# Kernel optimization log

Measured on AMD Instinct MI355X. Metric: run time of the kernel, lower is better.

The kernel has to match this reference:

```python
import jax, jax.numpy as jnp
import numpy as np

C_S, C_V, C_Z, C_OUT = 32, 8, 128, 128
IN_S, IN_V = 28, 37
N_RBF, N_POS = 64, 64
IN_Z = N_RBF * 25 + N_POS          # 1664 raw pairwise-dist RBF + positional feats
N_LAYERS, K = 4, 30
N_NODES = 1024
N_EDGES = N_NODES * K
WEIGHT_NUMEL = C_S*C_S + C_S*C_V + C_V*C_V + C_V*C_S + C_V*C_V  # 1664
LN_EPS = 1e-5
BN_EPS = 1e-5


def _ln(x, g, b):
    m = x.mean(-1, keepdims=True)
    v = x.var(-1, keepdims=True)
    return (x - m) / jnp.sqrt(v + LN_EPS) * g + b


def _tp(xs, xv, sh_s, sh_v, w):
    """FullyConnectedTensorProduct (32x0e+8x1e) x (0e+1e) -> (32x0e+8x1e), per-edge weights w [E, WEIGHT_NUMEL]."""
    E = w.shape[0]
    o = [0]
    def cut(n1, n2):
        ww = w[:, o[0]:o[0] + n1 * n2].reshape(E, n1, n2)
        o[0] += n1 * n2
        return ww
    w1 = cut(C_S, C_S)  # 0e x 0e -> 0e
    w2 = cut(C_S, C_V)  # 0e x 1e -> 1e
    w3 = cut(C_V, C_V)  # 1e x 0e -> 1e
    w4 = cut(C_V, C_S)  # 1e x 1e -> 0e (dot)
    w5 = cut(C_V, C_V)  # 1e x 1e -> 1e (cross)
    # path normalization: 1/sqrt(in1_mul * n_paths_to_output)
    a1 = 1.0 / np.sqrt(2 * C_S)
    a4 = 1.0 / np.sqrt(2 * C_V)
    a2 = 1.0 / np.sqrt(3 * C_S)
    a3 = 1.0 / np.sqrt(3 * C_V)
    a5 = a3
    out_s = a1 * jnp.einsum('e,ei,eij->ej', sh_s, xs, w1) \
          + (a4 / np.sqrt(3.0)) * jnp.einsum('eix,ex,eij->ej', xv, sh_v, w4)
    cross = jnp.cross(xv, sh_v[:, None, :])  # [E, C_V, 3]
    out_v = a2 * jnp.einsum('ei,eij,ex->ejx', xs, w2, sh_v) \
          + a3 * jnp.einsum('e,eix,eij->ejx', sh_s, xv, w3) \
          + (a5 / np.sqrt(2.0)) * jnp.einsum('eix,eij->ejx', cross, w5)
    return out_s, out_v


def _forward(node_raw, edge_raw, edge_vecs, rot,
             ee_w1, ee_b1, ee_w2, ee_b2, ee_w3, ee_b3, ee_ln_g, ee_ln_b,
             ne_ws, ne_wv,
             fc_w1, fc_b1, fc_w2, fc_b2, bn_g, bn_b, bn_vg,
             eu_lin, eu_w1, eu_b1, eu_w2, eu_b2, eu_w3, eu_b3, eu_ln_g, eu_ln_b,
             mu_w, mu_b, lv_w, lv_b, edge_index):
    N = node_raw.shape[0]
    dst, src = edge_index[0], edge_index[1]
    # spherical harmonics, lmax=1, 'component' normalization: Y0 = 1, Y1 = sqrt(3) * unit
    unit = edge_vecs / (jnp.linalg.norm(edge_vecs, axis=-1, keepdims=True) + 1e-8)
    sh_s = jnp.ones(edge_vecs.shape[0], node_raw.dtype)
    sh_v = np.sqrt(3.0) * unit
    # edge embed MLP + LN
    h = jax.nn.relu(edge_raw @ ee_w1 + ee_b1)
    h = jax.nn.relu(h @ ee_w2 + ee_b2)
    ef = _ln(h @ ee_w3 + ee_b3, ee_ln_g, ee_ln_b)
    # node embed: per-irrep (equivariant) linear 28x0e->32x0e, 37x1e->8x1e
    xs = node_raw[:, :IN_S] @ ne_ws
    xv = jnp.einsum('nix,ij->njx', node_raw[:, IN_S:].reshape(N, IN_V, 3), ne_wv)
    cnt = jnp.maximum(jax.ops.segment_sum(jnp.ones_like(src, node_raw.dtype), src, num_segments=N), 1.0)
    for l in range(N_LAYERS):
        # per-edge TP weights from edge features
        w = jax.nn.relu(ef @ fc_w1[l] + fc_b1[l]) @ fc_w2[l] + fc_b2[l]  # [E, WEIGHT_NUMEL]
        ms, mv = _tp(xs[dst], xv[dst], sh_s, sh_v, w)
        ags = jax.ops.segment_sum(ms, src, num_segments=N) / cnt[:, None]
        agv = jax.ops.segment_sum(mv, src, num_segments=N) / cnt[:, None, None]
        xs = xs + ags  # pad is a no-op: in/out irreps identical
        xv = xv + agv
        # e3nn-style BatchNorm (batch statistics)
        xs = (xs - xs.mean(0)) / jnp.sqrt(xs.var(0) + BN_EPS) * bn_g[l] + bn_b[l]
        fn = jnp.mean(jnp.sum(xv ** 2, -1), 0) / 3.0  # per-channel mean component norm
        xv = xv / jnp.sqrt(fn + BN_EPS)[None, :, None] * bn_vg[l][None, :, None]
        # EdgeUpdate
        a = xs @ eu_lin[l]  # scalar part -> h_edge
        e_in = jnp.concatenate([a[dst], a[src], ef], -1)
        u = jax.nn.relu(e_in @ eu_w1[l] + eu_b1[l])
        u = jax.nn.relu(u @ eu_w2[l] + eu_b2[l])
        u = u @ eu_w3[l] + eu_b3[l]
        ef = _ln(ef + u, eu_ln_g[l], eu_ln_b[l])
    # scalarize vectors w.r.t. per-node frames: R^T v
    xv_loc = jnp.einsum('nxy,ncx->ncy', rot, xv)
    feat = jnp.concatenate([xs, xv_loc.reshape(N, -1)], -1)  # [N, 56]
    mu = feat @ mu_w + mu_b
    lv = feat @ lv_w + lv_b
    return jnp.stack([mu, lv])  # [2, N, C_OUT]


def setup_inputs() -> dict:
    key = jax.random.key(0)
    ks = iter(jax.random.split(key, 80))
    def nrm(shape, fan=None):
        s = 1.0 if fan is None else 1.0 / np.sqrt(fan)
        return jax.random.normal(next(ks), shape, jnp.float32) * s
    inp = {}
    inp['node_raw'] = nrm([N_NODES, IN_S + 3 * IN_V])
    inp['edge_raw'] = nrm([N_EDGES, IN_Z])
    inp['edge_vecs'] = nrm([N_EDGES, 3])
    inp['rot'] = jnp.linalg.qr(nrm([N_NODES, 3, 3]))[0]
    inp['edge_index'] = jax.random.randint(next(ks), (2, N_EDGES), 0, N_NODES, jnp.int32)
    inp['ee_w1'] = nrm([IN_Z, C_Z], IN_Z); inp['ee_b1'] = jnp.zeros([C_Z])
    inp['ee_w2'] = nrm([C_Z, C_Z], C_Z);   inp['ee_b2'] = jnp.zeros([C_Z])
    inp['ee_w3'] = nrm([C_Z, C_Z], C_Z);   inp['ee_b3'] = jnp.zeros([C_Z])
    inp['ee_ln_g'] = jnp.ones([C_Z]); inp['ee_ln_b'] = jnp.zeros([C_Z])
    inp['ne_ws'] = nrm([IN_S, C_S], IN_S)
    inp['ne_wv'] = nrm([IN_V, C_V], IN_V)
    L = N_LAYERS
    inp['fc_w1'] = nrm([L, C_Z, C_Z], C_Z); inp['fc_b1'] = jnp.zeros([L, C_Z])
    inp['fc_w2'] = nrm([L, C_Z, WEIGHT_NUMEL], C_Z); inp['fc_b2'] = jnp.zeros([L, WEIGHT_NUMEL])
    inp['bn_g'] = jnp.ones([L, C_S]); inp['bn_b'] = jnp.zeros([L, C_S]); inp['bn_vg'] = jnp.ones([L, C_V])
    inp['eu_lin'] = nrm([L, C_S, C_Z], C_S)
    inp['eu_w1'] = nrm([L, 3 * C_Z, C_Z], 3 * C_Z); inp['eu_b1'] = jnp.zeros([L, C_Z])
    inp['eu_w2'] = nrm([L, C_Z, C_Z], C_Z); inp['eu_b2'] = jnp.zeros([L, C_Z])
    inp['eu_w3'] = nrm([L, C_Z, C_Z], C_Z); inp['eu_b3'] = jnp.zeros([L, C_Z])
    inp['eu_ln_g'] = jnp.ones([L, C_Z]); inp['eu_ln_b'] = jnp.zeros([L, C_Z])
    D = C_S + 3 * C_V
    inp['mu_w'] = nrm([D, C_OUT], D); inp['mu_b'] = jnp.zeros([C_OUT])
    inp['lv_w'] = nrm([D, C_OUT], D); inp['lv_b'] = jnp.zeros([C_OUT])
    return inp


def reference(node_raw, edge_raw, edge_vecs, rot,
              ee_w1, ee_b1, ee_w2, ee_b2, ee_w3, ee_b3, ee_ln_g, ee_ln_b,
              ne_ws, ne_wv,
              fc_w1, fc_b1, fc_w2, fc_b2, bn_g, bn_b, bn_vg,
              eu_lin, eu_w1, eu_b1, eu_w2, eu_b2, eu_w3, eu_b3, eu_ln_g, eu_ln_b,
              mu_w, mu_b, lv_w, lv_b, edge_index):
    return _forward(node_raw, edge_raw, edge_vecs, rot,
                    ee_w1, ee_b1, ee_w2, ee_b2, ee_w3, ee_b3, ee_ln_g, ee_ln_b,
                    ne_ws, ne_wv,
                    fc_w1, fc_b1, fc_w2, fc_b2, bn_g, bn_b, bn_vg,
                    eu_lin, eu_w1, eu_b1, eu_w2, eu_b2, eu_w3, eu_b3, eu_ln_g, eu_ln_b,
                    mu_w, mu_b, lv_w, lv_b, edge_index)
```

## Files before the change

### kernel.cpp

```cpp
#include <hip/hip_runtime.h>
#include <hip/hip_bf16.h>

typedef __hip_bfloat16 bf16;
typedef __attribute__((ext_vector_type(8))) short s16x8;
typedef __attribute__((ext_vector_type(4))) float f32x4;

#define NN 1024
#define NE 30720
#define CS 32
#define CV 8
#define CZ 128
#define INS 28
#define INV 37
#define NRDIM 139
#define INZ 1664
#define WN 1664
#define NL 4

__device__ __forceinline__ float b2f(bf16 x) { return __bfloat162float(x); }
__device__ __forceinline__ bf16 f2b(float x) { return __float2bfloat16(x); }


template<int RELU, int AF32>
__global__ __launch_bounds__(256)
void gemm64(const void* __restrict__ Ap, const bf16* __restrict__ Bf,
            const float* __restrict__ bias, bf16* __restrict__ Cp,
            int M, int K)
{
    __shared__ __align__(16) bf16 la[64 * 40];
    const int bm = blockIdx.x * 64;
    const int tid = threadIdx.x;
    const int lane = tid & 63;
    const int wv = tid >> 6;
    const int lr = tid >> 1;
    const int lc = (tid & 1) * 16;
    const int l15 = lane & 15;
    const int quad = lane >> 4;
    const int K32 = K >> 5;
    f32x4 acc[4][2] = {};
    const bf16*  ga16 = (const bf16*) Ap + (size_t)(bm + lr) * K + lc;
    const float* ga32 = (const float*)Ap + (size_t)(bm + lr) * K + lc;
    for (int k0 = 0; k0 < K; k0 += 32) {
        union { bf16 h[16]; float4 q[2]; } pa;
        if (tid < 128) {
            if (AF32) {
                float4 f0 = *(const float4*)(ga32 + k0);
                float4 f1 = *(const float4*)(ga32 + k0 + 4);
                float4 f2 = *(const float4*)(ga32 + k0 + 8);
                float4 f3 = *(const float4*)(ga32 + k0 + 12);
                pa.h[0]=f2b(f0.x); pa.h[1]=f2b(f0.y); pa.h[2]=f2b(f0.z); pa.h[3]=f2b(f0.w);
                pa.h[4]=f2b(f1.x); pa.h[5]=f2b(f1.y); pa.h[6]=f2b(f1.z); pa.h[7]=f2b(f1.w);
                pa.h[8]=f2b(f2.x); pa.h[9]=f2b(f2.y); pa.h[10]=f2b(f2.z); pa.h[11]=f2b(f2.w);
                pa.h[12]=f2b(f3.x); pa.h[13]=f2b(f3.y); pa.h[14]=f2b(f3.z); pa.h[15]=f2b(f3.w);
            } else {
                pa.q[0] = *(const float4*)(ga16 + k0);
                pa.q[1] = *(const float4*)(ga16 + k0 + 8);
            }
        }
        s16x8 bfr[2];
#pragma unroll
        for (int ni = 0; ni < 2; ni++)
            bfr[ni] = *(const s16x8*)(Bf + (size_t)(((wv * 2 + ni) * K32 + (k0 >> 5)) * 512) + lane * 8);
        __syncthreads();
        if (tid < 128) {
            *(float4*)&la[lr * 40 + lc]     = pa.q[0];
            *(float4*)&la[lr * 40 + lc + 8] = pa.q[1];
        }
        __syncthreads();
        s16x8 af[4];
#pragma unroll
        for (int mi = 0; mi < 4; mi++)
            af[mi] = *(const s16x8*)&la[(mi * 16 + l15) * 40 + quad * 8];
#pragma unroll
        for (int mi = 0; mi < 4; mi++)
#pragma unroll
            for (int ni = 0; ni < 2; ni++)
                acc[mi][ni] = __builtin_amdgcn_mfma_f32_16x16x32_bf16(af[mi], bfr[ni], acc[mi][ni], 0, 0, 0);
    }
#pragma unroll
    for (int ni = 0; ni < 2; ni++) {
        const int col = wv * 32 + ni * 16 + l15;
        const float bv = bias[col];
#pragma unroll
        for (int mi = 0; mi < 4; mi++) {
            const int row0 = bm + mi * 16 + quad * 4;
#pragma unroll
            for (int r = 0; r < 4; r++) {
                float v = acc[mi][ni][r] + bv;
                if (RELU) v = fmaxf(v, 0.f);
                Cp[(size_t)(row0 + r) * CZ + col] = f2b(v);
            }
        }
    }
}

__global__ __launch_bounds__(256)
void mlp2(const bf16* __restrict__ A,
          const bf16* __restrict__ w2f, const float* __restrict__ b2,
          const bf16* __restrict__ w3f, const float* __restrict__ b3,
          const float* __restrict__ g, const float* __restrict__ bb,
          bf16* efb)
{
    __shared__ __align__(16) bf16 s_a[64 * 136];
    __shared__ __align__(16) bf16 s_u[64 * 136];
    __shared__ float s_o[64 * 132];
    const int bm = blockIdx.x * 64;
    const int t = threadIdx.x;
    const int lane = t & 63;
    const int wv = t >> 6;
    const int l15 = lane & 15;
    const int quad = lane >> 4;
    {
        int r = t >> 2, c0 = (t & 3) * 32;
        const float4* s4 = (const float4*)(A + (size_t)(bm + r) * CZ + c0);
        float4* d4 = (float4*)&s_a[r * 136 + c0];
        d4[0] = s4[0]; d4[1] = s4[1]; d4[2] = s4[2]; d4[3] = s4[3];
    }
    __syncthreads();
    s16x8 af[4][4];
#pragma unroll
    for (int mi = 0; mi < 4; mi++)
#pragma unroll
        for (int kk = 0; kk < 4; kk++)
            af[mi][kk] = *(const s16x8*)&s_a[(mi * 16 + l15) * 136 + kk * 32 + quad * 8];
#pragma unroll
    for (int s = 0; s < 2; s++) {
        int n = wv * 32 + s * 16 + l15;
        f32x4 acc[4] = {};
#pragma unroll
        for (int kk = 0; kk < 4; kk++) {
            s16x8 bfr = *(const s16x8*)(w2f + (size_t)(((wv * 2 + s) * 4 + kk) * 512) + lane * 8);
#pragma unroll
            for (int mi = 0; mi < 4; mi++)
                acc[mi] = __builtin_amdgcn_mfma_f32_16x16x32_bf16(af[mi][kk], bfr, acc[mi], 0, 0, 0);
        }
        float bv = b2[n];
#pragma unroll
        for (int mi = 0; mi < 4; mi++)
#pragma unroll
            for (int r = 0; r < 4; r++)
                s_u[(mi * 16 + quad * 4 + r) * 136 + n] = f2b(fmaxf(acc[mi][r] + bv, 0.f));
    }
    __syncthreads();
#pragma unroll
    for (int mi = 0; mi < 4; mi++)
#pragma unroll
        for (int kk = 0; kk < 4; kk++)
            af[mi][kk] = *(const s16x8*)&s_u[(mi * 16 + l15) * 136 + kk * 32 + quad * 8];
#pragma unroll
    for (int s = 0; s < 2; s++) {
        int n = wv * 32 + s * 16 + l15;
        f32x4 acc[4] = {};
#pragma unroll
        for (int kk = 0; kk < 4; kk++) {
            s16x8 bfr = *(const s16x8*)(w3f + (size_t)(((wv * 2 + s) * 4 + kk) * 512) + lane * 8);
#pragma unroll
            for (int mi = 0; mi < 4; mi++)
                acc[mi] = __builtin_amdgcn_mfma_f32_16x16x32_bf16(af[mi][kk], bfr, acc[mi], 0, 0, 0);
        }
        float bv = b3[n];
#pragma unroll
        for (int mi = 0; mi < 4; mi++)
#pragma unroll
            for (int r = 0; r < 4; r++)
                s_o[(mi * 16 + quad * 4 + r) * 132 + n] = acc[mi][r] + bv;
    }
    __syncthreads();
    {
        int row = wv * 16 + (lane >> 2);
        int q = lane & 3;
        int col0 = q * 32;
        size_t gbase = (size_t)(bm + row) * CZ;
        float s = 0.f, s2 = 0.f;
        for (int i = 0; i < 32; i++) {
            float x = s_o[row * 132 + col0 + i];
            s += x; s2 += x * x;
        }
        s  += __shfl_xor(s, 1);  s2 += __shfl_xor(s2, 1);
        s  += __shfl_xor(s, 2);  s2 += __shfl_xor(s2, 2);
        float mean = s * (1.f / 128.f);
        float var  = s2 * (1.f / 128.f) - mean * mean;
        float rstd = rsqrtf(var + 1e-5f);
        for (int i = 0; i < 32; i++) {
            int col = col0 + i;
            float x = s_o[row * 132 + col];
            efb[gbase + col] = f2b((x - mean) * rstd * g[col] + bb[col]);
        }
    }
}

__global__ __launch_bounds__(256)
void eu_fused(bf16* __restrict__ efb,
              const float* __restrict__ adg, const float* __restrict__ asg,
              const int* __restrict__ ei,
              const bf16* __restrict__ w1cf, const float* __restrict__ b1,
              const bf16* __restrict__ w2f, const float* __restrict__ b2,
              const bf16* __restrict__ w3f, const float* __restrict__ b3,
              const float* __restrict__ g, const float* __restrict__ bb)
{
    __shared__ __align__(16) bf16 s_a[64 * 136];
    __shared__ __align__(16) bf16 s_u1[64 * 136];
    __shared__ __align__(16) float s_go[64 * 132];
    bf16* const s_u2 = (bf16*)s_go;
    const int bm = blockIdx.x * 64;
    const int t = threadIdx.x;
    const int lane = t & 63;
    const int wv = t >> 6;
    const int l15 = lane & 15;
    const int quad = lane >> 4;
    {
        int r = t >> 2, c0 = (t & 3) * 32;
        const float4* s4 = (const float4*)(efb + (size_t)(bm + r) * CZ + c0);
        float4* d4 = (float4*)&s_a[r * 136 + c0];
        d4[0] = s4[0]; d4[1] = s4[1]; d4[2] = s4[2]; d4[3] = s4[3];
        int dst = ei[bm + r], src = ei[NE + bm + r];
        const float4* pd = (const float4*)(adg + (size_t)dst * CZ + c0);
        const float4* ps = (const float4*)(asg + (size_t)src * CZ + c0);
        float4* dg = (float4*)&s_go[r * 132 + c0];
#pragma unroll
        for (int k = 0; k < 8; k++) {
            float4 va = pd[k], vb = ps[k];
            dg[k] = make_float4(va.x + vb.x, va.y + vb.y, va.z + vb.z, va.w + vb.w);
        }
    }
    __syncthreads();
    {
        s16x8 af[4][4];
#pragma unroll
        for (int mi = 0; mi < 4; mi++)
#pragma unroll
            for (int kk = 0; kk < 4; kk++)
                af[mi][kk] = *(const s16x8*)&s_a[(mi * 16 + l15) * 136 + kk * 32 + quad * 8];
#pragma unroll
        for (int s = 0; s < 2; s++) {
            int n = wv * 32 + s * 16 + l15;
            f32x4 acc[4] = {};
#pragma unroll
            for (int kk = 0; kk < 4; kk++) {
                s16x8 bfr = *(const s16x8*)(w1cf + (size_t)(((wv * 2 + s) * 4 + kk) * 512) + lane * 8);
#pragma unroll
                for (int mi = 0; mi < 4; mi++)
                    acc[mi] = __builtin_amdgcn_mfma_f32_16x16x32_bf16(af[mi][kk], bfr, acc[mi], 0, 0, 0);
            }
            float bv = b1[n];
#pragma unroll
            for (int mi = 0; mi < 4; mi++)
#pragma unroll
                for (int r = 0; r < 4; r++) {
                    int e = mi * 16 + quad * 4 + r;
                    s_u1[e * 136 + n] = f2b(fmaxf(acc[mi][r] + bv + s_go[e * 132 + n], 0.f));
                }
        }
    }
    __syncthreads();
    {
        s16x8 af[4][4];
#pragma unroll
        for (int mi = 0; mi < 4; mi++)
#pragma unroll
            for (int kk = 0; kk < 4; kk++)
                af[mi][kk] = *(const s16x8*)&s_u1[(mi * 16 + l15) * 136 + kk * 32 + quad * 8];
#pragma unroll
        for (int s = 0; s < 2; s++) {
            int n = wv * 32 + s * 16 + l15;
            f32x4 acc[4] = {};
#pragma unroll
            for (int kk = 0; kk < 4; kk++) {
                s16x8 bfr = *(const s16x8*)(w2f + (size_t)(((wv * 2 + s) * 4 + kk) * 512) + lane * 8);
#pragma unroll
                for (int mi = 0; mi < 4; mi++)
                    acc[mi] = __builtin_amdgcn_mfma_f32_16x16x32_bf16(af[mi][kk], bfr, acc[mi], 0, 0, 0);
            }
            float bv = b2[n];
#pragma unroll
            for (int mi = 0; mi < 4; mi++)
#pragma unroll
                for (int r = 0; r < 4; r++)
                    s_u2[(mi * 16 + quad * 4 + r) * 136 + n] = f2b(fmaxf(acc[mi][r] + bv, 0.f));
        }
    }
    __syncthreads();
    {
        s16x8 af[4][4];
#pragma unroll
        for (int mi = 0; mi < 4; mi++)
#pragma unroll
            for (int kk = 0; kk < 4; kk++)
                af[mi][kk] = *(const s16x8*)&s_u2[(mi * 16 + l15) * 136 + kk * 32 + quad * 8];
        __syncthreads();
#pragma unroll
        for (int s = 0; s < 2; s++) {
            int n = wv * 32 + s * 16 + l15;
            f32x4 acc[4] = {};
#pragma unroll
            for (int kk = 0; kk < 4; kk++) {
                s16x8 bfr = *(const s16x8*)(w3f + (size_t)(((wv * 2 + s) * 4 + kk) * 512) + lane * 8);
#pragma unroll
                for (int mi = 0; mi < 4; mi++)
                    acc[mi] = __builtin_amdgcn_mfma_f32_16x16x32_bf16(af[mi][kk], bfr, acc[mi], 0, 0, 0);
            }
            float bv = b3[n];
#pragma unroll
            for (int mi = 0; mi < 4; mi++)
#pragma unroll
                for (int r = 0; r < 4; r++) {
                    int e = mi * 16 + quad * 4 + r;
                    s_go[e * 132 + n] = acc[mi][r] + bv + b2f(s_a[e * 136 + n]);
                }
        }
    }
    __syncthreads();
    {
        int row = wv * 16 + (lane >> 2);
        int q = lane & 3;
        int col0 = q * 32;
        size_t gbase = (size_t)(bm + row) * CZ;
        float s = 0.f, s2 = 0.f;
        for (int i = 0; i < 32; i++) {
            float x = s_go[row * 132 + col0 + i];
            s += x; s2 += x * x;
        }
        s  += __shfl_xor(s, 1);  s2 += __shfl_xor(s2, 1);
        s  += __shfl_xor(s, 2);  s2 += __shfl_xor(s2, 2);
        float mean = s * (1.f / 128.f);
        float var  = s2 * (1.f / 128.f) - mean * mean;
        float rstd = rsqrtf(var + 1e-5f);
        for (int i = 0; i < 32; i++) {
            int col = col0 + i;
            float x = s_go[row * 132 + col];
            efb[gbase + col] = f2b((x - mean) * rstd * g[col] + bb[col]);
        }
    }
}

__global__ __launch_bounds__(256, 2)
void fc2_tp(const bf16* __restrict__ ef,
            const bf16* __restrict__ w1f, const float* __restrict__ b1,
            const bf16* __restrict__ w2f, const float* __restrict__ b2,
            const int* __restrict__ ei, const float* __restrict__ edge_vecs,
            const float* __restrict__ xs, const float* __restrict__ xv,
            float* __restrict__ tp_s, float* __restrict__ tp_v)
{
    __shared__ __align__(16) bf16 s_a[64 * 136];
    __shared__ __align__(16) bf16 s_h[64 * 136];
    __shared__ __align__(16) float s_xsT[32][64];
    __shared__ __align__(16) float s_xvT[24][64];
    __shared__ __align__(16) float s_crT[24][64];
    __shared__ __align__(16) float s_y4T[8][64];
    __shared__ __align__(16) float s_b2[WN];
    __shared__ float s_shv[64][3];
    __shared__ int s_dst[64];
    __shared__ float s_os[64][32];
    __shared__ float s_ov[64][24];
    const int be = blockIdx.x * 64;
    const int t = threadIdx.x;
    const int lane = t & 63;
    const int wv = t >> 6;
    const int l15 = lane & 15;
    const int quad = lane >> 4;
    const int q4 = quad * 4;

    if (t < 64) {
        int e = be + t;
        s_dst[t] = ei[e];
        float vx = edge_vecs[e * 3 + 0];
        float vy = edge_vecs[e * 3 + 1];
        float vz = edge_vecs[e * 3 + 2];
        float sc = 1.7320508075688772f / (sqrtf(vx * vx + vy * vy + vz * vz) + 1e-8f);
        s_shv[t][0] = vx * sc; s_shv[t][1] = vy * sc; s_shv[t][2] = vz * sc;
    }
    for (int i = t; i < 64 * 32; i += 256) ((float*)s_os)[i] = 0.f;
    for (int i = t; i < 64 * 24; i += 256) ((float*)s_ov)[i] = 0.f;
    for (int i = t; i < WN; i += 256) s_b2[i] = b2[i];
    {
        int r = t >> 2, c0 = (t & 3) * 32;
        const float4* s4 = (const float4*)(ef + (size_t)(be + r) * CZ + c0);
        float4* d4 = (float4*)&s_a[r * 136 + c0];
        d4[0] = s4[0]; d4[1] = s4[1]; d4[2] = s4[2]; d4[3] = s4[3];
    }
    __syncthreads();
    for (int i = t; i < 64 * 32; i += 256) { int e = i & 63, c = i >> 6; s_xsT[c][e] = xs[s_dst[e] * CS + c]; }
    for (int i = t; i < 64 * 24; i += 256) { int e = i & 63, c = i >> 6; s_xvT[c][e] = xv[s_dst[e] * 24 + c]; }
    __syncthreads();
    for (int i2 = t; i2 < 512; i2 += 256) {
        int e = i2 & 63, i = i2 >> 6;
        float h0 = s_shv[e][0], h1 = s_shv[e][1], h2 = s_shv[e][2];
        float x0 = s_xvT[i * 3 + 0][e], x1 = s_xvT[i * 3 + 1][e], x2 = s_xvT[i * 3 + 2][e];
        s_y4T[i][e] = 1.1547005383792515f * (x0 * h0 + x1 * h1 + x2 * h2);
        s_crT[i * 3 + 0][e] = 0.7071067811865476f * (x1 * h2 - x2 * h1);
        s_crT[i * 3 + 1][e] = 0.7071067811865476f * (x2 * h0 - x0 * h2);
        s_crT[i * 3 + 2][e] = 0.7071067811865476f * (x0 * h1 - x1 * h0);
    }
    {
        s16x8 af1[4][4];
#pragma unroll
        for (int mi = 0; mi < 4; mi++)
#pragma unroll
            for (int kk = 0; kk < 4; kk++)
                af1[mi][kk] = *(const s16x8*)&s_a[(mi * 16 + l15) * 136 + kk * 32 + quad * 8];
#pragma unroll
        for (int s = 0; s < 2; s++) {
            int n = wv * 32 + s * 16 + l15;
            f32x4 acc[4] = {};
#pragma unroll
            for (int kk = 0; kk < 4; kk++) {
                s16x8 bfr = *(const s16x8*)(w1f + (size_t)(((wv * 2 + s) * 4 + kk) * 512) + lane * 8);
#pragma unroll
                for (int mi = 0; mi < 4; mi++)
                    acc[mi] = __builtin_amdgcn_mfma_f32_16x16x32_bf16(af1[mi][kk], bfr, acc[mi], 0, 0, 0);
            }
            float bv = b1[n];
#pragma unroll
            for (int mi = 0; mi < 4; mi++)
#pragma unroll
                for (int r = 0; r < 4; r++)
                    s_h[(mi * 16 + quad * 4 + r) * 136 + n] = f2b(fmaxf(acc[mi][r] + bv, 0.f));
        }
    }
    __syncthreads();
    s16x8 af[4][4];
#pragma unroll
    for (int mi = 0; mi < 4; mi++)
#pragma unroll
        for (int kk = 0; kk < 4; kk++)
            af[mi][kk] = *(const s16x8*)&s_h[(mi * 16 + l15) * 136 + kk * 32 + quad * 8];
    float os[4][4] = {}, sv2[4][4] = {}, ov0[4][4] = {}, ov1[4][4] = {}, ov2[4][4] = {};
    const int ib = l15 >> 3;
    for (int nt = wv; nt < 104; nt += 4) {
        const float bv = s_b2[nt * 16 + l15];
        const bf16* wb = w2f + (size_t)(nt * 4) * 512 + lane * 8;
        s16x8 bfr[4];
#pragma unroll
        for (int kk = 0; kk < 4; kk++)
            bfr[kk] = *(const s16x8*)(wb + kk * 512);
        f32x4 ac[4] = {};
#pragma unroll
        for (int kk = 0; kk < 4; kk++)
#pragma unroll
            for (int mi = 0; mi < 4; mi++)
                ac[mi] = __builtin_amdgcn_mfma_f32_16x16x32_bf16(af[mi][kk], bfr[kk], ac[mi], 0, 0, 0);
        if (nt < 64) {
            const int i = nt >> 1;
#pragma unroll
            for (int mi = 0; mi < 4; mi++) {
                float4 f = *(const float4*)&s_xsT[i][mi * 16 + q4];
                os[mi][0] += (ac[mi][0] + bv) * f.x; os[mi][1] += (ac[mi][1] + bv) * f.y;
                os[mi][2] += (ac[mi][2] + bv) * f.z; os[mi][3] += (ac[mi][3] + bv) * f.w;
            }
        } else if (nt < 80) {
            const int i = (nt - 64) * 2 + ib;
#pragma unroll
            for (int mi = 0; mi < 4; mi++) {
                float4 f = *(const float4*)&s_xsT[i][mi * 16 + q4];
                sv2[mi][0] += (ac[mi][0] + bv) * f.x; sv2[mi][1] += (ac[mi][1] + bv) * f.y;
                sv2[mi][2] += (ac[mi][2] + bv) * f.z; sv2[mi][3] += (ac[mi][3] + bv) * f.w;
            }
        } else if (nt < 84) {
            const int i0 = ((nt - 80) * 2 + ib) * 3;
#pragma unroll
            for (int mi = 0; mi < 4; mi++) {
                float4 f0 = *(const float4*)&s_xvT[i0 + 0][mi * 16 + q4];
                float4 f1 = *(const float4*)&s_xvT[i0 + 1][mi * 16 + q4];
                float4 f2 = *(const float4*)&s_xvT[i0 + 2][mi * 16 + q4];
                float w0 = ac[mi][0] + bv, w1 = ac[mi][1] + bv, w2 = ac[mi][2] + bv, w3 = ac[mi][3] + bv;
                ov0[mi][0] += w0 * f0.x; ov0[mi][1] += w1 * f0.y; ov0[mi][2] += w2 * f0.z; ov0[mi][3] += w3 * f0.w;
                ov1[mi][0] += w0 * f1.x; ov1[mi][1] += w1 * f1.y; ov1[mi][2] += w2 * f1.z; ov1[mi][3] += w3 * f1.w;
                ov2[mi][0] += w0 * f2.x; ov2[mi][1] += w1 * f2.y; ov2[mi][2] += w2 * f2.z; ov2[mi][3] += w3 * f2.w;
            }
        } else if (nt < 100) {
            const int i = (nt - 84) >> 1;
#pragma unroll
            for (int mi = 0; mi < 4; mi++) {
                float4 f = *(const float4*)&s_y4T[i][mi * 16 + q4];
                os[mi][0] += (ac[mi][0] + bv) * f.x; os[mi][1] += (ac[mi][1] + bv) * f.y;
                os[mi][2] += (ac[mi][2] + bv) * f.z; os[mi][3] += (ac[mi][3] + bv) * f.w;
            }
        } else {
            const int i0 = ((nt - 100) * 2 + ib) * 3;
#pragma unroll
            for (int mi = 0; mi < 4; mi++) {
                float4 f0 = *(const float4*)&s_crT[i0 + 0][mi * 16 + q4];
                float4 f1 = *(const float4*)&s_crT[i0 + 1][mi * 16 + q4];
                float4 f2 = *(const float4*)&s_crT[i0 + 2][mi * 16 + q4];
                float w0 = ac[mi][0] + bv, w1 = ac[mi][1] + bv, w2 = ac[mi][2] + bv, w3 = ac[mi][3] + bv;
                ov0[mi][0] += w0 * f0.x; ov0[mi][1] += w1 * f0.y; ov0[mi][2] += w2 * f0.z; ov0[mi][3] += w3 * f0.w;
                ov1[mi][0] += w0 * f1.x; ov1[mi][1] += w1 * f1.y; ov1[mi][2] += w2 * f1.z; ov1[mi][3] += w3 * f1.w;
                ov2[mi][0] += w0 * f2.x; ov2[mi][1] += w1 * f2.y; ov2[mi][2] += w2 * f2.z; ov2[mi][3] += w3 * f2.w;
            }
        }
    }
    {
        const int jo = (wv & 1) * 16 + l15;
        const int jv3 = (l15 & 7) * 3;
#pragma unroll
        for (int mi = 0; mi < 4; mi++)
#pragma unroll
            for (int r = 0; r < 4; r++) {
                int e = mi * 16 + quad * 4 + r;
                atomicAdd(&s_os[e][jo], os[mi][r]);
                float sv = 0.5f * sv2[mi][r];
                atomicAdd(&s_ov[e][jv3 + 0], ov0[mi][r] + s_shv[e][0] * sv);
                atomicAdd(&s_ov[e][jv3 + 1], ov1[mi][r] + s_shv[e][1] * sv);
                atomicAdd(&s_ov[e][jv3 + 2], ov2[mi][r] + s_shv[e][2] * sv);
            }
    }
    __syncthreads();
    for (int i = t; i < 64 * 32; i += 256) {
        int e = i >> 5, d = i & 31;
        tp_s[(size_t)(be + e) * 32 + d] = s_os[e][d] * 0.125f;
    }
    for (int i = t; i < 64 * 24; i += 256) {
        int e = i / 24, d = i - e * 24;
        tp_v[(size_t)(be + e) * 24 + d] = s_ov[e][d] * 0.2041241452319315f;
    }
}

__global__ __launch_bounds__(1024)
void scan_csr(const int* __restrict__ cnt, int* __restrict__ row_start,
              int* __restrict__ fillpos, float* __restrict__ icnt)
{
    __shared__ int tmp[1024];
    int t = threadIdx.x;
    int v = cnt[t];
    tmp[t] = v;
    __syncthreads();
    for (int o = 1; o < 1024; o <<= 1) {
        int x = (t >= o) ? tmp[t - o] : 0;
        __syncthreads();
        tmp[t] += x;
        __syncthreads();
    }
    int excl = tmp[t] - v;
    row_start[t] = excl;
    fillpos[t] = excl;
    if (t == 1023) row_start[1024] = tmp[1023];
    icnt[t] = 1.0f / (float)(v > 1 ? v : 1);
}

__global__ void fill_perm(const int* __restrict__ ei, int* __restrict__ fillpos,
                          int* __restrict__ perm)
{
    int e = blockIdx.x * 256 + threadIdx.x;
    if (e < NE) {
        int s = ei[NE + e];
        int p = atomicAdd(&fillpos[s], 1);
        perm[p] = e;
    }
}

__global__ __launch_bounds__(64)
void aggregate(const float* __restrict__ tp_s, const float* __restrict__ tp_v,
               const int* __restrict__ perm, const int* __restrict__ row_start,
               const float* __restrict__ icnt,
               float* __restrict__ ags, float* __restrict__ agv)
{
    __shared__ int s_e[64];
    const int n = blockIdx.x, t = threadIdx.x;
    const int s = row_start[n], epe = row_start[n + 1];
    float acc = 0.f;
    for (int k0 = s; k0 < epe; k0 += 64) {
        int kk = k0 + t;
        s_e[t] = (kk < epe) ? perm[kk] : 0;
        __syncthreads();
        int m = epe - k0; if (m > 64) m = 64;
        for (int j = 0; j < m; j++) {
            int e = s_e[j];
            acc += (t < 32) ? tp_s[(size_t)e * 32 + t]
                            : tp_v[(size_t)e * 24 + (t - 32)];
        }
        __syncthreads();
    }
    acc *= icnt[n];
    if (t < 32) ags[n * CS + t] = acc;
    else if (t < 56) agv[n * 24 + (t - 32)] = acc;
}

__device__ __forceinline__ void fragseg(int i, int R, int C,
                                        const float* __restrict__ s, bf16* __restrict__ d)
{
    int l = i / (R * C);
    int rem = i - l * R * C;
    int k = rem / C;
    int n = rem - k * C;
    int dst = ((n >> 4) * (R >> 5) + (k >> 5)) * 512 + ((k >> 3) & 3) * 128 + (n & 15) * 8 + (k & 7);
    d[(size_t)l * R * C + dst] = f2b(s[i]);
}

__global__ void transpose_all(const float* __restrict__ p0, const float* __restrict__ p1,
                              const float* __restrict__ p2, const float* __restrict__ p3,
                              const float* __restrict__ p4, const float* __restrict__ p5,
                              const float* __restrict__ p6, const float* __restrict__ p7,
                              bf16* d0, bf16* d1, bf16* d2, bf16* d3,
                              bf16* d4, bf16* d5, bf16* d6, bf16* d7)
{
    int i = blockIdx.x * 256 + threadIdx.x;
    const int S0 = INZ * CZ;
    const int S1 = CZ * CZ;
    const int S2 = CZ * CZ;
    const int S3 = NL * CZ * CZ;
    const int S4 = NL * CZ * WN;
    const int S5 = NL * 384 * CZ;
    const int S6 = NL * CZ * CZ;
    const int S7 = NL * CZ * CZ;
    if (i < S0) { fragseg(i, INZ, CZ, p0, d0); return; } i -= S0;
    if (i < S1) { fragseg(i, CZ, CZ, p1, d1); return; }  i -= S1;
    if (i < S2) { fragseg(i, CZ, CZ, p2, d2); return; }  i -= S2;
    if (i < S3) { fragseg(i, CZ, CZ, p3, d3); return; }  i -= S3;
    if (i < S4) { fragseg(i, CZ, WN, p4, d4); return; }  i -= S4;
    if (i < S5) {
        int l = i / (384 * CZ);
        int rem = i - l * (384 * CZ);
        int k = rem / CZ, n = rem - k * CZ;
        if (k >= 256) {
            int k2 = k - 256;
            int dst = ((n >> 4) * (CZ >> 5) + (k2 >> 5)) * 512 + ((k2 >> 3) & 3) * 128 + (n & 15) * 8 + (k2 & 7);
            d5[(size_t)l * CZ * CZ + dst] = f2b(p5[i]);
        }
        return;
    } i -= S5;
    if (i < S6) { fragseg(i, CZ, CZ, p6, d6); return; }  i -= S6;
    if (i < S7) { fragseg(i, CZ, CZ, p7, d7); return; }
}

__global__ __launch_bounds__(256)
void fold_f(const float* __restrict__ eu_lin, const float* __restrict__ eu_w1,
            float* __restrict__ Fw)
{
    int b = blockIdx.x, t = threadIdx.x;
    int l = b >> 1, part = b & 1;
    const float* L = eu_lin + (size_t)l * CS * CZ;
    const float* W = eu_w1 + (size_t)l * 384 * CZ + (size_t)part * CZ * CZ;
    float* out = Fw + (size_t)b * CS * CZ;
    for (int idx = t; idx < CS * CZ; idx += 256) {
        int i = idx >> 7, n = idx & 127;
        float acc = 0.f;
        for (int k = 0; k < CZ; k++)
            acc += L[i * CZ + k] * W[k * CZ + n];
        out[idx] = acc;
    }
}

__global__ __launch_bounds__(128)
void adas(const float* __restrict__ xs, const float* __restrict__ Fd,
          const float* __restrict__ Fs, float* __restrict__ adg, float* __restrict__ asg)
{
    __shared__ float sxs[32];
    int n = blockIdx.x, t = threadIdx.x;
    if (t < 32) sxs[t] = xs[n * CS + t];
    __syncthreads();
    float a = 0.f, b = 0.f;
    for (int i = 0; i < 32; i++) {
        float x = sxs[i];
        a += x * Fd[i * CZ + t];
        b += x * Fs[i * CZ + t];
    }
    adg[(size_t)n * CZ + t] = a;
    asg[(size_t)n * CZ + t] = b;
}

__global__ __launch_bounds__(64)
void node_embed(const float* __restrict__ node_raw, const float* __restrict__ ne_ws,
                const float* __restrict__ ne_wv, float* __restrict__ xs, float* __restrict__ xv)
{
    int n = blockIdx.x, t = threadIdx.x;
    const float* nr = node_raw + (size_t)n * NRDIM;
    if (t < 32) {
        float acc = 0.f;
        for (int i = 0; i < INS; i++) acc += nr[i] * ne_ws[i * CS + t];
        xs[n * CS + t] = acc;
    } else if (t < 56) {
        int t2 = t - 32, j = t2 / 3, x = t2 - 3 * (t2 / 3);
        float acc = 0.f;
        for (int i = 0; i < INV; i++) acc += nr[INS + i * 3 + x] * ne_wv[i * CV + j];
        xv[n * 24 + t2] = acc;
    }
}

__global__ void count_src(const int* __restrict__ ei, int* __restrict__ cnt)
{
    int e = blockIdx.x * 256 + threadIdx.x;
    if (e < NE) atomicAdd(&cnt[ei[NE + e]], 1);
}

__global__ __launch_bounds__(256)
void bnfused(float* __restrict__ xs, float* __restrict__ xv,
             const float* __restrict__ ags, const float* __restrict__ agv,
             const float* __restrict__ g, const float* __restrict__ b,
             const float* __restrict__ vg)
{
    __shared__ float red[8];
    __shared__ float stat[2];
    int c = blockIdx.x, t = threadIdx.x;
    if (c < 32) {
        float s = 0.f, s2 = 0.f;
        for (int n = t; n < NN; n += 256) {
            float v = xs[n * CS + c] + ags[n * CS + c];
            s += v; s2 += v * v;
        }
        for (int o = 32; o > 0; o >>= 1) { s += __shfl_down(s, o); s2 += __shfl_down(s2, o); }
        int w = t >> 6;
        if ((t & 63) == 0) { red[w * 2] = s; red[w * 2 + 1] = s2; }
        __syncthreads();
        if (t == 0) {
            float S = red[0] + red[2] + red[4] + red[6];
            float S2 = red[1] + red[3] + red[5] + red[7];
            float mean = S * (1.f / NN);
            float var = S2 * (1.f / NN) - mean * mean;
            stat[0] = mean;
            stat[1] = rsqrtf(var + 1e-5f);
        }
        __syncthreads();
        float mean = stat[0], rstd = stat[1], gg = g[c], bb = b[c];
        for (int n = t; n < NN; n += 256) {
            int ix = n * CS + c;
            float v = xs[ix] + ags[ix];
            xs[ix] = (v - mean) * rstd * gg + bb;
        }
    } else {
        int c2 = c - 32;
        float s = 0.f;
        for (int n = t; n < NN; n += 256) {
            float v0 = xv[n * 24 + c2 * 3 + 0] + agv[n * 24 + c2 * 3 + 0];
            float v1 = xv[n * 24 + c2 * 3 + 1] + agv[n * 24 + c2 * 3 + 1];
            float v2 = xv[n * 24 + c2 * 3 + 2] + agv[n * 24 + c2 * 3 + 2];
            s += v0 * v0 + v1 * v1 + v2 * v2;
        }
        for (int o = 32; o > 0; o >>= 1) s += __shfl_down(s, o);
        int w = t >> 6;
        if ((t & 63) == 0) red[w] = s;
        __syncthreads();
        if (t == 0) {
            float fn = (red[0] + red[1] + red[2] + red[3]) * (1.f / (3.f * NN));
            stat[0] = vg[c2] * rsqrtf(fn + 1e-5f);
        }
        __syncthreads();
        float scale = stat[0];
        for (int n = t; n < NN; n += 256) {
            for (int x = 0; x < 3; x++) {
                int ix = n * 24 + c2 * 3 + x;
                xv[ix] = (xv[ix] + agv[ix]) * scale;
            }
        }
    }
}

__global__ __launch_bounds__(128)
void final_out(const float* __restrict__ xs, const float* __restrict__ xv,
               const float* __restrict__ rot,
               const float* __restrict__ mu_w, const float* __restrict__ mu_b,
               const float* __restrict__ lv_w, const float* __restrict__ lv_b,
               float* __restrict__ out)
{
    __shared__ float feat[56];
    int n = blockIdx.x, t = threadIdx.x;
    if (t < 32) feat[t] = xs[n * CS + t];
    else if (t < 56) {
        int t2 = t - 32, c = t2 / 3, y = t2 - 3 * (t2 / 3);
        float acc = 0.f;
        for (int x = 0; x < 3; x++)
            acc += rot[n * 9 + x * 3 + y] * xv[n * 24 + c * 3 + x];
        feat[t] = acc;
    }
    __syncthreads();
    float mu = mu_b[t], lv = lv_b[t];
    for (int d = 0; d < 56; d++) {
        float f = feat[d];
        mu += f * mu_w[d * 128 + t];
        lv += f * lv_w[d * 128 + t];
    }
    out[(size_t)n * 128 + t] = mu;
    out[(size_t)NN * 128 + (size_t)n * 128 + t] = lv;
}

extern "C" void kernel_launch(void* const* d_in, const int* in_sizes, int n_in,
                              void* d_out, int out_size, void* d_ws, size_t ws_size,
                              hipStream_t stream)
{
    (void)in_sizes; (void)n_in; (void)out_size; (void)ws_size;
    const float* node_raw  = (const float*)d_in[0];
    const float* edge_raw  = (const float*)d_in[1];
    const float* edge_vecs = (const float*)d_in[2];
    const float* rot       = (const float*)d_in[3];
    const int*   ei        = (const int*  )d_in[4];
    const float* ee_w1 = (const float*)d_in[5];
    const float* ee_b1 = (const float*)d_in[6];
    const float* ee_w2 = (const float*)d_in[7];
    const float* ee_b2 = (const float*)d_in[8];
    const float* ee_w3 = (const float*)d_in[9];
    const float* ee_b3 = (const float*)d_in[10];
    const float* ee_ln_g = (const float*)d_in[11];
    const float* ee_ln_b = (const float*)d_in[12];
    const float* ne_ws = (const float*)d_in[13];
    const float* ne_wv = (const float*)d_in[14];
    const float* fc_w1 = (const float*)d_in[15];
    const float* fc_b1 = (const float*)d_in[16];
    const float* fc_w2 = (const float*)d_in[17];
    const float* fc_b2 = (const float*)d_in[18];
    const float* bn_g  = (const float*)d_in[19];
    const float* bn_b  = (const float*)d_in[20];
    const float* bn_vg = (const float*)d_in[21];
    const float* eu_lin = (const float*)d_in[22];
    const float* eu_w1 = (const float*)d_in[23];
    const float* eu_b1 = (const float*)d_in[24];
    const float* eu_w2 = (const float*)d_in[25];
    const float* eu_b2 = (const float*)d_in[26];
    const float* eu_w3 = (const float*)d_in[27];
    const float* eu_b3 = (const float*)d_in[28];
    const float* eu_ln_g = (const float*)d_in[29];
    const float* eu_ln_b = (const float*)d_in[30];
    const float* mu_w = (const float*)d_in[31];
    const float* mu_b = (const float*)d_in[32];
    const float* lv_w = (const float*)d_in[33];
    const float* lv_b = (const float*)d_in[34];

    char* ws = (char*)d_ws;
    size_t off = 0;
    auto alloc = [&](size_t bytes) -> void* {
        void* p = ws + off;
        off += (bytes + 255) & ~(size_t)255;
        return p;
    };
    bf16*  ef_b  = (bf16*) alloc((size_t)NE * CZ * 2);
    bf16*  buf_a = (bf16*) alloc((size_t)NE * CZ * 2);
    float* xs    = (float*)alloc((size_t)NN * CS * 4);
    float* xv    = (float*)alloc((size_t)NN * 24 * 4);
    float* ags   = (float*)alloc((size_t)NN * CS * 4);
    float* agv   = (float*)alloc((size_t)NN * 24 * 4);
    int*   cnti  = (int*)  alloc((size_t)NN * 4);
    float* icnt  = (float*)alloc((size_t)NN * 4);
    float* adg   = (float*)alloc((size_t)NN * CZ * 4);
    float* asg   = (float*)alloc((size_t)NN * CZ * 4);
    float* Fw    = (float*)alloc((size_t)NL * 2 * CS * CZ * 4);
    float* tp_s  = (float*)alloc((size_t)NE * 32 * 4);
    float* tp_v  = (float*)alloc((size_t)NE * 24 * 4 + 64);
    int*   perm  = (int*)  alloc((size_t)NE * 4);
    int*   row_start = (int*)alloc((size_t)(NN + 1) * 4);
    int*   fillpos   = (int*)alloc((size_t)NN * 4);
    bf16* ee_w1t = (bf16*)alloc((size_t)INZ * CZ * 2);
    bf16* ee_w2t = (bf16*)alloc((size_t)CZ * CZ * 2);
    bf16* ee_w3t = (bf16*)alloc((size_t)CZ * CZ * 2);
    bf16* fc_w1t = (bf16*)alloc((size_t)NL * CZ * CZ * 2);
    bf16* fc_w2t = (bf16*)alloc((size_t)NL * WN * CZ * 2);
    bf16* eu_w1ct = (bf16*)alloc((size_t)NL * CZ * CZ * 2);
    bf16* eu_w2t = (bf16*)alloc((size_t)NL * CZ * CZ * 2);
    bf16* eu_w3t = (bf16*)alloc((size_t)NL * CZ * CZ * 2);

    const int TRN = INZ*CZ + 2*CZ*CZ + NL*CZ*CZ + NL*CZ*WN + NL*384*CZ + 2*NL*CZ*CZ;
    transpose_all<<<(TRN + 255) / 256, 256, 0, stream>>>(
        ee_w1, ee_w2, ee_w3, fc_w1, fc_w2, eu_w1, eu_w2, eu_w3,
        ee_w1t, ee_w2t, ee_w3t, fc_w1t, fc_w2t, eu_w1ct, eu_w2t, eu_w3t);
    fold_f<<<NL * 2, 256, 0, stream>>>(eu_lin, eu_w1, Fw);

    node_embed<<<NN, 64, 0, stream>>>(node_raw, ne_ws, ne_wv, xs, xv);
    hipMemsetAsync(cnti, 0, NN * 4, stream);
    count_src<<<NE / 256, 256, 0, stream>>>(ei, cnti);
    scan_csr<<<1, 1024, 0, stream>>>(cnti, row_start, fillpos, icnt);
    fill_perm<<<NE / 256, 256, 0, stream>>>(ei, fillpos, perm);

    const int GE = NE / 64;
    gemm64<1, 1><<<GE, 256, 0, stream>>>(edge_raw, ee_w1t, ee_b1, buf_a, NE, INZ);
    mlp2<<<GE, 256, 0, stream>>>(buf_a, ee_w2t, ee_b2, ee_w3t, ee_b3, ee_ln_g, ee_ln_b, ef_b);

    for (int l = 0; l < NL; l++) {
        fc2_tp<<<GE, 256, 0, stream>>>(
            ef_b, fc_w1t + (size_t)l * CZ * CZ, fc_b1 + l * CZ,
            fc_w2t + (size_t)l * WN * CZ, fc_b2 + l * WN,
            ei, edge_vecs, xs, xv, tp_s, tp_v);
        aggregate<<<NN, 64, 0, stream>>>(tp_s, tp_v, perm, row_start, icnt, ags, agv);
        bnfused<<<40, 256, 0, stream>>>(xs, xv, ags, agv,
                                        bn_g + l * CS, bn_b + l * CS, bn_vg + l * CV);
        adas<<<NN, 128, 0, stream>>>(xs, Fw + (size_t)(l * 2) * CS * CZ,
                                     Fw + (size_t)(l * 2 + 1) * CS * CZ, adg, asg);
        eu_fused<<<GE, 256, 0, stream>>>(
            ef_b, adg, asg, ei,
            eu_w1ct + (size_t)l * CZ * CZ, eu_b1 + l * CZ,
            eu_w2t + (size_t)l * CZ * CZ, eu_b2 + l * CZ,
            eu_w3t + (size_t)l * CZ * CZ, eu_b3 + l * CZ,
            eu_ln_g + l * CZ, eu_ln_b + l * CZ);
    }

    final_out<<<NN, 128, 0, stream>>>(xs, xv, rot, mu_w, mu_b, lv_w, lv_b, (float*)d_out);
}
```

Measured before the change: 877.4 us.

## Software-pipeline weight and A-tile loads in GEMM and fused edge kernels

```diff
diff --git a/kernel.cpp b/kernel.cpp
--- a/kernel.cpp
+++ b/kernel.cpp
@@ -40,33 +40,41 @@
     f32x4 acc[4][2] = {};
     const bf16*  ga16 = (const bf16*) Ap + (size_t)(bm + lr) * K + lc;
     const float* ga32 = (const float*)Ap + (size_t)(bm + lr) * K + lc;
-    for (int k0 = 0; k0 < K; k0 += 32) {
-        union { bf16 h[16]; float4 q[2]; } pa;
+
+    auto loadA = [&](float4 (&q)[4], int k0) {
         if (tid < 128) {
             if (AF32) {
-                float4 f0 = *(const float4*)(ga32 + k0);
-                float4 f1 = *(const float4*)(ga32 + k0 + 4);
-                float4 f2 = *(const float4*)(ga32 + k0 + 8);
-                float4 f3 = *(const float4*)(ga32 + k0 + 12);
-                pa.h[0]=f2b(f0.x); pa.h[1]=f2b(f0.y); pa.h[2]=f2b(f0.z); pa.h[3]=f2b(f0.w);
-                pa.h[4]=f2b(f1.x); pa.h[5]=f2b(f1.y); pa.h[6]=f2b(f1.z); pa.h[7]=f2b(f1.w);
-                pa.h[8]=f2b(f2.x); pa.h[9]=f2b(f2.y); pa.h[10]=f2b(f2.z); pa.h[11]=f2b(f2.w);
-                pa.h[12]=f2b(f3.x); pa.h[13]=f2b(f3.y); pa.h[14]=f2b(f3.z); pa.h[15]=f2b(f3.w);
+                q[0] = *(const float4*)(ga32 + k0);
+                q[1] = *(const float4*)(ga32 + k0 + 4);
+                q[2] = *(const float4*)(ga32 + k0 + 8);
+                q[3] = *(const float4*)(ga32 + k0 + 12);
             } else {
-                pa.q[0] = *(const float4*)(ga16 + k0);
-                pa.q[1] = *(const float4*)(ga16 + k0 + 8);
-            }
-        }
-        s16x8 bfr[2];
+                q[0] = *(const float4*)(ga16 + k0);
+                q[1] = *(const float4*)(ga16 + k0 + 8);
+            }
+        }
+    };
+    auto storeA = [&](float4 (&q)[4]) {
+        if (tid < 128) {
+            if (AF32) {
+                union { bf16 h[16]; float4 v[2]; } pa;
+                const float* f = (const float*)q;
+#pragma unroll
+                for (int i = 0; i < 16; i++) pa.h[i] = f2b(f[i]);
+                *(float4*)&la[lr * 40 + lc]     = pa.v[0];
+                *(float4*)&la[lr * 40 + lc + 8] = pa.v[1];
+            } else {
+                *(float4*)&la[lr * 40 + lc]     = q[0];
+                *(float4*)&la[lr * 40 + lc + 8] = q[1];
+            }
+        }
+    };
+    auto loadB = [&](s16x8 (&B)[2], int k0) {
 #pragma unroll
         for (int ni = 0; ni < 2; ni++)
-            bfr[ni] = *(const s16x8*)(Bf + (size_t)(((wv * 2 + ni) * K32 + (k0 >> 5)) * 512) + lane * 8);
-        __syncthreads();
-        if (tid < 128) {
-            *(float4*)&la[lr * 40 + lc]     = pa.q[0];
-            *(float4*)&la[lr * 40 + lc + 8] = pa.q[1];
-        }
-        __syncthreads();
+            B[ni] = *(const s16x8*)(Bf + (size_t)(((wv * 2 + ni) * K32 + (k0 >> 5)) * 512) + lane * 8);
+    };
+    auto mmac = [&](s16x8 (&B)[2]) {
         s16x8 af[4];
 #pragma unroll
         for (int mi = 0; mi < 4; mi++)
@@ -75,7 +83,24 @@
         for (int mi = 0; mi < 4; mi++)
 #pragma unroll
             for (int ni = 0; ni < 2; ni++)
-                acc[mi][ni] = __builtin_amdgcn_mfma_f32_16x16x32_bf16(af[mi], bfr[ni], acc[mi][ni], 0, 0, 0);
+                acc[mi][ni] = __builtin_amdgcn_mfma_f32_16x16x32_bf16(af[mi], B[ni], acc[mi][ni], 0, 0, 0);
+    };
+
+    float4 qA[4], qB[4];
+    s16x8 bA[2], bB[2];
+    loadA(qA, 0); loadB(bA, 0);
+#pragma unroll 1
+    for (int k0 = 0; k0 < K; k0 += 64) {
+        loadA(qB, k0 + 32); loadB(bB, k0 + 32);
+        __syncthreads();
+        storeA(qA);
+        __syncthreads();
+        mmac(bA);
+        if (k0 + 64 < K) { loadA(qA, k0 + 64); loadB(bA, k0 + 64); }
+        __syncthreads();
+        storeA(qB);
+        __syncthreads();
+        mmac(bB);
     }
 #pragma unroll
     for (int ni = 0; ni < 2; ni++) {
@@ -110,6 +135,15 @@
     const int wv = t >> 6;
     const int l15 = lane & 15;
     const int quad = lane >> 4;
+    s16x8 w2r[2][4], w3r[2][4];
+#pragma unroll
+    for (int s = 0; s < 2; s++)
+#pragma unroll
+        for (int kk = 0; kk < 4; kk++) {
+            const size_t o = (size_t)(((wv * 2 + s) * 4 + kk) * 512) + lane * 8;
+            w2r[s][kk] = *(const s16x8*)(w2f + o);
+            w3r[s][kk] = *(const s16x8*)(w3f + o);
+        }
     {
         int r = t >> 2, c0 = (t & 3) * 32;
         const float4* s4 = (const float4*)(A + (size_t)(bm + r) * CZ + c0);
@@ -128,12 +162,10 @@
         int n = wv * 32 + s * 16 + l15;
         f32x4 acc[4] = {};
 #pragma unroll
-        for (int kk = 0; kk < 4; kk++) {
-            s16x8 bfr = *(const s16x8*)(w2f + (size_t)(((wv * 2 + s) * 4 + kk) * 512) + lane * 8);
+        for (int kk = 0; kk < 4; kk++)
 #pragma unroll
             for (int mi = 0; mi < 4; mi++)
-                acc[mi] = __builtin_amdgcn_mfma_f32_16x16x32_bf16(af[mi][kk], bfr, acc[mi], 0, 0, 0);
-        }
+                acc[mi] = __builtin_amdgcn_mfma_f32_16x16x32_bf16(af[mi][kk], w2r[s][kk], acc[mi], 0, 0, 0);
         float bv = b2[n];
 #pragma unroll
         for (int mi = 0; mi < 4; mi++)
@@ -152,12 +184,10 @@
         int n = wv * 32 + s * 16 + l15;
         f32x4 acc[4] = {};
 #pragma unroll
-        for (int kk = 0; kk < 4; kk++) {
-            s16x8 bfr = *(const s16x8*)(w3f + (size_t)(((wv * 2 + s) * 4 + kk) * 512) + lane * 8);
+        for (int kk = 0; kk < 4; kk++)
 #pragma unroll
             for (int mi = 0; mi < 4; mi++)
-                acc[mi] = __builtin_amdgcn_mfma_f32_16x16x32_bf16(af[mi][kk], bfr, acc[mi], 0, 0, 0);
-        }
+                acc[mi] = __builtin_amdgcn_mfma_f32_16x16x32_bf16(af[mi][kk], w3r[s][kk], acc[mi], 0, 0, 0);
         float bv = b3[n];
 #pragma unroll
         for (int mi = 0; mi < 4; mi++)
@@ -208,6 +238,15 @@
     const int wv = t >> 6;
     const int l15 = lane & 15;
     const int quad = lane >> 4;
+    s16x8 w1r[2][4], w2r[2][4];
+#pragma unroll
+    for (int s = 0; s < 2; s++)
+#pragma unroll
+        for (int kk = 0; kk < 4; kk++) {
+            const size_t o = (size_t)(((wv * 2 + s) * 4 + kk) * 512) + lane * 8;
+            w1r[s][kk] = *(const s16x8*)(w1cf + o);
+            w2r[s][kk] = *(const s16x8*)(w2f + o);
+        }
     {
         int r = t >> 2, c0 = (t & 3) * 32;
         const float4* s4 = (const float4*)(efb + (size_t)(bm + r) * CZ + c0);
@@ -224,6 +263,7 @@
         }
     }
     __syncthreads();
+    s16x8 w3r[2][4];
     {
         s16x8 af[4][4];
 #pragma unroll
@@ -231,17 +271,20 @@
 #pragma unroll
             for (int kk = 0; kk < 4; kk++)
                 af[mi][kk] = *(const s16x8*)&s_a[(mi * 16 + l15) * 136 + kk * 32 + quad * 8];
+#pragma unroll
+        for (int s = 0; s < 2; s++)
+#pragma unroll
+            for (int kk = 0; kk < 4; kk++)
+                w3r[s][kk] = *(const s16x8*)(w3f + (size_t)(((wv * 2 + s) * 4 + kk) * 512) + lane * 8);
 #pragma unroll
         for (int s = 0; s < 2; s++) {
             int n = wv * 32 + s * 16 + l15;
             f32x4 acc[4] = {};
 #pragma unroll
-            for (int kk = 0; kk < 4; kk++) {
-                s16x8 bfr = *(const s16x8*)(w1cf + (size_t)(((wv * 2 + s) * 4 + kk) * 512) + lane * 8);
+            for (int kk = 0; kk < 4; kk++)
 #pragma unroll
                 for (int mi = 0; mi < 4; mi++)
-                    acc[mi] = __builtin_amdgcn_mfma_f32_16x16x32_bf16(af[mi][kk], bfr, acc[mi], 0, 0, 0);
-            }
+                    acc[mi] = __builtin_amdgcn_mfma_f32_16x16x32_bf16(af[mi][kk], w1r[s][kk], acc[mi], 0, 0, 0);
             float bv = b1[n];
 #pragma unroll
             for (int mi = 0; mi < 4; mi++)
@@ -265,12 +308,10 @@
             int n = wv * 32 + s * 16 + l15;
             f32x4 acc[4] = {};
 #pragma unroll
-            for (int kk = 0; kk < 4; kk++) {
-                s16x8 bfr = *(const s16x8*)(w2f + (size_t)(((wv * 2 + s) * 4 + kk) * 512) + lane * 8);
+            for (int kk = 0; kk < 4; kk++)
 #pragma unroll
                 for (int mi = 0; mi < 4; mi++)
-                    acc[mi] = __builtin_amdgcn_mfma_f32_16x16x32_bf16(af[mi][kk], bfr, acc[mi], 0, 0, 0);
-            }
+                    acc[mi] = __builtin_amdgcn_mfma_f32_16x16x32_bf16(af[mi][kk], w2r[s][kk], acc[mi], 0, 0, 0);
             float bv = b2[n];
 #pragma unroll
             for (int mi = 0; mi < 4; mi++)
@@ -293,12 +334,10 @@
             int n = wv * 32 + s * 16 + l15;
             f32x4 acc[4] = {};
 #pragma unroll
-            for (int kk = 0; kk < 4; kk++) {
-                s16x8 bfr = *(const s16x8*)(w3f + (size_t)(((wv * 2 + s) * 4 + kk) * 512) + lane * 8);
+            for (int kk = 0; kk < 4; kk++)
 #pragma unroll
                 for (int mi = 0; mi < 4; mi++)
-                    acc[mi] = __builtin_amdgcn_mfma_f32_16x16x32_bf16(af[mi][kk], bfr, acc[mi], 0, 0, 0);
-            }
+                    acc[mi] = __builtin_amdgcn_mfma_f32_16x16x32_bf16(af[mi][kk], w3r[s][kk], acc[mi], 0, 0, 0);
             float bv = b3[n];
 #pragma unroll
             for (int mi = 0; mi < 4; mi++)
@@ -426,13 +465,14 @@
             af[mi][kk] = *(const s16x8*)&s_h[(mi * 16 + l15) * 136 + kk * 32 + quad * 8];
     float os[4][4] = {}, sv2[4][4] = {}, ov0[4][4] = {}, ov1[4][4] = {}, ov2[4][4] = {};
     const int ib = l15 >> 3;
-    for (int nt = wv; nt < 104; nt += 4) {
+
+    auto loadw = [&](s16x8 (&B)[4], int NT) {
+        const bf16* wb = w2f + (size_t)(NT * 4) * 512 + lane * 8;
+#pragma unroll
+        for (int kk = 0; kk < 4; kk++) B[kk] = *(const s16x8*)(wb + kk * 512);
+    };
+    auto consume = [&](int nt, s16x8 (&bfr)[4]) {
         const float bv = s_b2[nt * 16 + l15];
-        const bf16* wb = w2f + (size_t)(nt * 4) * 512 + lane * 8;
-        s16x8 bfr[4];
-#pragma unroll
-        for (int kk = 0; kk < 4; kk++)
-            bfr[kk] = *(const s16x8*)(wb + kk * 512);
         f32x4 ac[4] = {};
 #pragma unroll
         for (int kk = 0; kk < 4; kk++)
@@ -487,6 +527,20 @@
                 ov1[mi][0] += w0 * f1.x; ov1[mi][1] += w1 * f1.y; ov1[mi][2] += w2 * f1.z; ov1[mi][3] += w3 * f1.w;
                 ov2[mi][0] += w0 * f2.x; ov2[mi][1] += w1 * f2.y; ov2[mi][2] += w2 * f2.z; ov2[mi][3] += w3 * f2.w;
             }
+        }
+    };
+
+    {
+        s16x8 bA[4], bB[4];
+        int nt = wv;
+        loadw(bA, nt);
+#pragma unroll 1
+        for (int p = 0; p < 13; p++) {
+            loadw(bB, nt + 4);
+            consume(nt, bA);
+            if (p < 12) loadw(bA, nt + 8);
+            consume(nt + 4, bB);
+            nt += 8;
         }
     }
     {
```

After: 869.1 us. Within noise of the previous version (-1.0%).
